# Kernel optimization log

Hardware: AMD Instinct MI355X
Metric: run time of the kernel (lower is better)

The kernel has to match this reference:

```python
import jax, jax.numpy as jnp
import numpy as np

B, T = 2, 512
E, NH, HD, V, P, L, KER, BLOCK = 768, 12, 64, 256, 4, 4, 16, 512
SCALE = HD ** -0.5


def _ln(x, g, b, eps=1e-5):
    m = jnp.mean(x, -1, keepdims=True)
    v = jnp.mean((x - m) ** 2, -1, keepdims=True)
    return (x - m) * jax.lax.rsqrt(v + eps) * g + b


def _rope_tables(n):
    inv = 1.0 / (10000.0 ** (jnp.arange(0, HD, 2, dtype=jnp.float32) / HD))
    f = jnp.arange(n, dtype=jnp.float32)[:, None] * inv[None, :]
    return jnp.cos(f), jnp.sin(f)


def _rope(x, cos, sin):
    # rotate over last two dims (positions, HD); split-half RoPE as in source
    h = x.shape[-1] // 2
    x1, x2 = x[..., :h], x[..., h:]
    return jnp.concatenate([x1 * cos - x2 * sin, x1 * sin + x2 * cos], axis=-1)


def _patch_attn(x, qkv_w, S):
    # x: [B,T,E]; sliding-window patch attention, step=1
    Bb, Tt, _ = x.shape
    q, k, v = jnp.split(x @ qkv_w, 3, axis=-1)
    heads = lambda t: t.reshape(Bb, Tt, NH, HD).transpose(0, 2, 1, 3)  # [B,NH,T,HD]
    q, k, v = heads(q), heads(k), heads(v)
    cos, sin = _rope_tables(Tt)
    q = _rope(q, cos, sin)
    k = _rope(k, cos, sin)
    # prefix: full causal attention over first S tokens
    sc = jnp.einsum('bnqh,bnkh->bnqk', q[:, :, :S], k[:, :, :S]) * SCALE
    mask = jnp.tril(jnp.ones((S, S), dtype=bool))
    sc = jnp.where(mask, sc, jnp.float32(-jnp.inf))
    out = jnp.einsum('bnqk,bnkh->bnqh', jax.nn.softmax(sc, axis=-1), v[:, :, :S])
    if Tt > S:
        # query t (t>=S) attends keys [t-S+1, t] (mask_sliding is all-ones for step=1)
        idx = jnp.arange(Tt - S)[:, None] + 1 + jnp.arange(S)[None, :]  # [T-S,S]
        kw = k[:, :, idx]  # [B,NH,T-S,S,HD]
        vw = v[:, :, idx]
        qs = q[:, :, S:]   # [B,NH,T-S,HD]
        sw = jnp.einsum('bnth,bntsh->bnts', qs, kw) * SCALE
        ow = jnp.einsum('bnts,bntsh->bnth', jax.nn.softmax(sw, axis=-1), vw)
        out = jnp.concatenate([out, ow], axis=2)
    return out.transpose(0, 2, 1, 3).reshape(Bb, Tt, NH * HD)


def _sa_block(x, ln0g, ln0b, ln1g, ln1b, qkv_w, proj_w, proj_b, w1, b1, w2, b2):
    # x: [B,T,P,V]; full (unmasked) attention over the P prediction slots
    Bb, Tt, Pp, _ = x.shape
    h = _ln(x, ln0g, ln0b)
    q, k, v = jnp.split(h @ qkv_w, 3, axis=-1)
    heads = lambda t: t.reshape(Bb, Tt, Pp, NH, HD).transpose(0, 1, 3, 2, 4)  # [B,T,NH,P,HD]
    q, k, v = heads(q), heads(k), heads(v)
    cos, sin = _rope_tables(Pp)
    q = _rope(q, cos, sin)
    k = _rope(k, cos, sin)
    sc = jnp.einsum('btnph,btnqh->btnpq', q, k) * SCALE
    o = jnp.einsum('btnpq,btnqh->btnph', jax.nn.softmax(sc, axis=-1), v)
    o = o.transpose(0, 1, 3, 2, 4).reshape(Bb, Tt, Pp, NH * HD)
    x = x + (o @ proj_w + proj_b)
    h2 = _ln(x, ln1g, ln1b)
    ff = jax.nn.gelu(h2 @ w1 + b1, approximate=False) @ w2 + b2
    return x + ff


def _forward(tokens, emb, blk_ln0_g, blk_ln0_b, blk_ln1_g, blk_ln1_b, blk_qkv_w,
             blk_ff_w1, blk_ff_b1, blk_ff_w2, blk_ff_b2, fin_ln_g, fin_ln_b,
             head_w, head_b, sa_ln0_g, sa_ln0_b, sa_ln1_g, sa_ln1_b, sa_qkv_w,
             sa_proj_w, sa_proj_b, sa_ff_w1, sa_ff_b1, sa_ff_w2, sa_ff_b2):
    x0 = emb[tokens]  # [B,T,E]
    x = x0
    for i in range(L):
        S = min(KER * 2 ** i, BLOCK)
        h = _ln(x, blk_ln0_g[i], blk_ln0_b[i])
        x = x + _patch_attn(h, blk_qkv_w[i], S)
        h2 = _ln(x, blk_ln1_g[i], blk_ln1_b[i])
        x = x + (jax.nn.gelu(h2 @ blk_ff_w1[i] + blk_ff_b1[i], approximate=False)
                 @ blk_ff_w2[i] + blk_ff_b2[i])
    x = x0 + x  # Golu: x = token_embedding(x); x = x + blocks(x)
    x = _ln(x, fin_ln_g, fin_ln_b)
    logits = (x @ head_w + head_b).reshape(B, T, P, V)
    logits = _sa_block(logits, sa_ln0_g, sa_ln0_b, sa_ln1_g, sa_ln1_b, sa_qkv_w,
                       sa_proj_w, sa_proj_b, sa_ff_w1, sa_ff_b1, sa_ff_w2, sa_ff_b2)
    return logits[:, :, 0, :]  # [B,T,V] (y is None path)


def setup_inputs() -> dict:
    key = jax.random.key(0)
    ks = jax.random.split(key, 12)
    w = lambda k, sh: jax.random.normal(k, sh, dtype=jnp.float32) * 0.02
    return {
        'tokens': jax.random.randint(ks[0], (B, T), 0, V),
        'emb': w(ks[1], (V, E)),
        'blk_ln0_g': jnp.ones((L, E), jnp.float32),
        'blk_ln0_b': jnp.zeros((L, E), jnp.float32),
        'blk_ln1_g': jnp.ones((L, E), jnp.float32),
        'blk_ln1_b': jnp.zeros((L, E), jnp.float32),
        'blk_qkv_w': w(ks[2], (L, E, 3 * E)),
        'blk_ff_w1': w(ks[3], (L, E, 4 * E)),
        'blk_ff_b1': jnp.zeros((L, 4 * E), jnp.float32),
        'blk_ff_w2': w(ks[4], (L, 4 * E, E)),
        'blk_ff_b2': jnp.zeros((L, E), jnp.float32),
        'fin_ln_g': jnp.ones((E,), jnp.float32),
        'fin_ln_b': jnp.zeros((E,), jnp.float32),
        'head_w': w(ks[5], (E, V * P)),
        'head_b': jnp.zeros((V * P,), jnp.float32),
        'sa_ln0_g': jnp.ones((V,), jnp.float32),
        'sa_ln0_b': jnp.zeros((V,), jnp.float32),
        'sa_ln1_g': jnp.ones((V,), jnp.float32),
        'sa_ln1_b': jnp.zeros((V,), jnp.float32),
        'sa_qkv_w': w(ks[6], (V, 3 * E)),
        'sa_proj_w': w(ks[7], (E, V)),
        'sa_proj_b': jnp.zeros((V,), jnp.float32),
        'sa_ff_w1': w(ks[8], (V, 4 * V)),
        'sa_ff_b1': jnp.zeros((4 * V,), jnp.float32),
        'sa_ff_w2': w(ks[9], (4 * V, V)),
        'sa_ff_b2': jnp.zeros((V,), jnp.float32),
    }


def reference(tokens, emb, blk_ln0_g, blk_ln0_b, blk_ln1_g, blk_ln1_b, blk_qkv_w,
              blk_ff_w1, blk_ff_b1, blk_ff_w2, blk_ff_b2, fin_ln_g, fin_ln_b,
              head_w, head_b, sa_ln0_g, sa_ln0_b, sa_ln1_g, sa_ln1_b, sa_qkv_w,
              sa_proj_w, sa_proj_b, sa_ff_w1, sa_ff_b1, sa_ff_w2, sa_ff_b2):
    return _forward(tokens, emb, blk_ln0_g, blk_ln0_b, blk_ln1_g, blk_ln1_b,
                    blk_qkv_w, blk_ff_w1, blk_ff_b1, blk_ff_w2, blk_ff_b2,
                    fin_ln_g, fin_ln_b, head_w, head_b, sa_ln0_g, sa_ln0_b,
                    sa_ln1_g, sa_ln1_b, sa_qkv_w, sa_proj_w, sa_proj_b,
                    sa_ff_w1, sa_ff_b1, sa_ff_w2, sa_ff_b2)
```

## Files before the change

kernel.cpp:

```cpp
#include <hip/hip_runtime.h>
#include <hip/hip_bf16.h>
#include <cstdint>
#include <cstddef>

#define BB    2
#define TSEQ  512
#define EDIM  768
#define NHEAD 12
#define HDIM  64
#define VDIM  256
#define PDIM  4
#define NROW  (BB*TSEQ)
#define NROW2 (BB*TSEQ*PDIM)

typedef __attribute__((ext_vector_type(8))) short short8;
typedef __attribute__((ext_vector_type(4))) short short4v;
typedef __attribute__((ext_vector_type(4))) float floatx4;

__device__ __forceinline__ float gelu_f(float v){
    return 0.5f * v * (1.0f + erff(v * 0.70710678118654752f));
}
__device__ __forceinline__ float b2f(short s){
    unsigned u = ((unsigned)(unsigned short)s) << 16;
    float f; __builtin_memcpy(&f, &u, 4); return f;
}
__device__ __forceinline__ short f2bs(float v){
    __hip_bfloat16 h = __float2bfloat16(v);
    short s; __builtin_memcpy(&s, &h, 2); return s;
}
__device__ __forceinline__ void gload16(const void* g, void* l){
    __builtin_amdgcn_global_load_lds((const __attribute__((address_space(1))) void*)g,
                                     (__attribute__((address_space(3))) void*)l, 16, 0, 0);
}

#define WAITN(n) asm volatile("s_waitcnt vmcnt(" #n ")" ::: "memory")
#define WAIT_STAGE(rem, full, half)                         \
    do{ if((rem) >= 2)      WAITN(full);                    \
        else if((rem) == 1) WAITN(half);                    \
        else                WAITN(0);                       \
        asm volatile("s_barrier" ::: "memory"); }while(0)
#define WAIT_STAGE8T(rem)                                   \
    do{ if((rem) >= 6)      WAITN(12);                      \
        else if((rem) == 5) WAITN(10);                      \
        else if((rem) == 4) WAITN(8);                       \
        else if((rem) == 3) WAITN(6);                       \
        else if((rem) == 2) WAITN(4);                       \
        else if((rem) == 1) WAITN(2);                       \
        else                WAITN(0);                       \
        asm volatile("s_barrier" ::: "memory"); }while(0)

struct WD2 { const float* in; __hip_bfloat16* out; int K; int N; int nt; };
struct WDs { WD2 d[17]; };

__global__ __launch_bounds__(256) void wconv_all(WDs a)
{
    int id = blockIdx.x;
    int i = 0;
    while(i < 16 && id >= a.d[i].nt){ id -= a.d[i].nt; i++; }
    WD2 w = a.d[i];
    const int tx = w.N / 128;
    const int n0 = (id % tx) * 128, k0 = (id / tx) * 128;
    __shared__ short t[128*128];
    {
        const int c4 = (threadIdx.x & 31) * 4;
        const int r0 = threadIdx.x >> 5;
        #pragma unroll
        for(int half = 0; half < 2; half++){
            float4 v[8];
            #pragma unroll
            for(int it = 0; it < 8; it++){
                int r = r0 + it*8 + half*64;
                v[it] = *(const float4*)(w.in + (size_t)(k0 + r) * w.N + n0 + c4);
            }
            #pragma unroll
            for(int it = 0; it < 8; it++){
                int r = r0 + it*8 + half*64;
                int nswz = c4 ^ (((r >> 3) & 15) << 2);
                short4v o;
                o[0] = f2bs(v[it].x); o[1] = f2bs(v[it].y);
                o[2] = f2bs(v[it].z); o[3] = f2bs(v[it].w);
                *(short4v*)&t[r*128 + nswz] = o;
            }
        }
    }
    __syncthreads();
    {
        const int k8 = (threadIdx.x & 15) * 8;
        const int nr = threadIdx.x >> 4;
        const int swz = (k8 >> 3) << 2;
        #pragma unroll
        for(int pass = 0; pass < 8; pass++){
            int n = nr + pass*16;
            int nswz = n ^ swz;
            short8 o;
            #pragma unroll
            for(int j = 0; j < 8; j++) o[j] = t[(k8 + j)*128 + nswz];
            *(short8*)((short*)w.out + (size_t)(n0 + n) * w.K + k0 + k8) = o;
        }
    }
}

template<int EPI>
__global__ __launch_bounds__(256) void gemm64q(
    const short* __restrict__ A, const short* __restrict__ Bt,
    const float* __restrict__ bias, __hip_bfloat16* __restrict__ Cout,
    __hip_bfloat16* __restrict__ qrb, __hip_bfloat16* __restrict__ krb,
    __hip_bfloat16* __restrict__ vvb,
    const float* __restrict__ rc, const float* __restrict__ rs,
    int M, int N, int K)
{
    alignas(16) __shared__ short As[4*64*32];
    alignas(16) __shared__ short Bs[4*64*32];
    const int tid  = threadIdx.x;
    const int lane = tid & 63;
    const int wave = tid >> 6;
    const int bm = blockIdx.y * 64, bn = blockIdx.x * 64;
    const int wm = wave * 16;
    const int quad = lane >> 4, l16 = lane & 15;

    floatx4 acc[4];
    #pragma unroll
    for(int j = 0; j < 4; j++) acc[j] = floatx4{0.f, 0.f, 0.f, 0.f};

    const int r  = tid >> 2;
    const int c8 = (tid & 3) * 8;
    const int ldsoff = (tid & 192) * 16;

    auto issue = [&](int k0, int cur){
        char* ab = (char*)As + cur*4096 + ldsoff;
        char* bb = (char*)Bs + cur*4096 + ldsoff;
        gload16(A  + (size_t)(bm + r) * K + k0 + c8, ab);
        gload16(Bt + (size_t)(bn + r) * K + k0 + c8, bb);
    };

    const int niter = K >> 5;
    issue(0, 0); issue(32, 1); issue(64, 2);
    for(int it = 0; it < niter; it++){
        WAIT_STAGE(niter - 1 - it, 4, 2);
        if(it + 3 < niter) issue((it + 3) << 5, (it + 3) & 3);
        const short* Ab = As + (it & 3) * 2048;
        const short* Bb = Bs + (it & 3) * 2048;
        short8 af = *(const short8*)&Ab[(wm + l16)*32 + quad*8];
        short8 bfr[4];
        #pragma unroll
        for(int j = 0; j < 4; j++)
            bfr[j] = *(const short8*)&Bb[(j*16 + l16)*32 + quad*8];
        #pragma unroll
        for(int j = 0; j < 4; j++)
            acc[j] = __builtin_amdgcn_mfma_f32_16x16x32_bf16(af, bfr[j], acc[j], 0, 0, 0);
    }

    if(EPI == 2){
        const int region = bn / 768;
        const int h = (bn % 768) >> 6;
        #pragma unroll
        for(int rr = 0; rr < 4; rr++){
            int row = bm + wm + quad*4 + rr;
            int t = row & (TSEQ-1), b = row >> 9;
            float a0 = acc[0][rr], a1 = acc[1][rr];
            float a2 = acc[2][rr], a3 = acc[3][rr];
            size_t dbase = ((size_t)(b*NHEAD + h)*TSEQ + t)*HDIM;
            if(region == 2){
                vvb[dbase + l16]      = __float2bfloat16(a0);
                vvb[dbase + 16 + l16] = __float2bfloat16(a1);
                vvb[dbase + 32 + l16] = __float2bfloat16(a2);
                vvb[dbase + 48 + l16] = __float2bfloat16(a3);
            }else{
                float c0 = rc[t*32 + l16],      s0 = rs[t*32 + l16];
                float c1 = rc[t*32 + 16 + l16], s1 = rs[t*32 + 16 + l16];
                __hip_bfloat16* dst = (region == 0) ? qrb : krb;
                dst[dbase + l16]      = __float2bfloat16(a0*c0 - a2*s0);
                dst[dbase + 16 + l16] = __float2bfloat16(a1*c1 - a3*s1);
                dst[dbase + 32 + l16] = __float2bfloat16(a0*s0 + a2*c0);
                dst[dbase + 48 + l16] = __float2bfloat16(a1*s1 + a3*c1);
            }
        }
        return;
    }

    if(EPI == 3){
        const int region = bn / 768;
        #pragma unroll
        for(int rr = 0; rr < 4; rr++){
            int row = bm + wm + quad*4 + rr;
            float a0 = acc[0][rr], a1 = acc[1][rr];
            float a2 = acc[2][rr], a3 = acc[3][rr];
            size_t rowb = (size_t)row * N + bn;
            if(region == 2){
                Cout[rowb + l16]      = __float2bfloat16(a0);
                Cout[rowb + 16 + l16] = __float2bfloat16(a1);
                Cout[rowb + 32 + l16] = __float2bfloat16(a2);
                Cout[rowb + 48 + l16] = __float2bfloat16(a3);
            }else{
                int p = row & 3;
                float c0 = rc[p*32 + l16],      s0 = rs[p*32 + l16];
                float c1 = rc[p*32 + 16 + l16], s1 = rs[p*32 + 16 + l16];
                Cout[rowb + l16]      = __float2bfloat16(a0*c0 - a2*s0);
                Cout[rowb + 16 + l16] = __float2bfloat16(a1*c1 - a3*s1);
                Cout[rowb + 32 + l16] = __float2bfloat16(a0*s0 + a2*c0);
                Cout[rowb + 48 + l16] = __float2bfloat16(a1*s1 + a3*c1);
            }
        }
        return;
    }

    #pragma unroll
    for(int j = 0; j < 4; j++){
        int col = bn + j*16 + l16;
        float bv = bias ? bias[col] : 0.f;
        #pragma unroll
        for(int rr = 0; rr < 4; rr++){
            int row = bm + wm + quad*4 + rr;
            float v = acc[j][rr] + bv;
            v = gelu_f(v);
            Cout[(size_t)row * N + col] = __float2bfloat16(v);
        }
    }
}

template<int RESID, int OUTC>
__global__ __launch_bounds__(256) void gemm64t(
    const short* __restrict__ A, const short* __restrict__ Bt,
    const float* __restrict__ bias, const float* __restrict__ resid,
    float* __restrict__ Cf, float* __restrict__ outp, int M, int N, int K)
{
    alignas(16) __shared__ short As[8*64*32];
    alignas(16) __shared__ short Bs[8*64*32];
    const int tid  = threadIdx.x;
    const int lane = tid & 63;
    const int wave = tid >> 6;
    const int bm = blockIdx.y * 64, bn = blockIdx.x * 64;
    const int wm = (wave >> 1) * 32, wn = (wave & 1) * 32;
    const int quad = lane >> 4, l16 = lane & 15;

    floatx4 acc[2][2];
    #pragma unroll
    for(int i = 0; i < 2; i++)
        #pragma unroll
        for(int j = 0; j < 2; j++)
            acc[i][j] = floatx4{0.f, 0.f, 0.f, 0.f};

    const int r  = tid >> 2;
    const int c8 = (tid & 3) * 8;
    const int ldsoff = (tid & 192) * 16;

    auto issue = [&](int k0, int cur){
        char* ab = (char*)As + cur*4096 + ldsoff;
        char* bb = (char*)Bs + cur*4096 + ldsoff;
        gload16(A  + (size_t)(bm + r) * K + k0 + c8, ab);
        gload16(Bt + (size_t)(bn + r) * K + k0 + c8, bb);
    };

    const int niter = K >> 5;
    issue(0, 0); issue(32, 1); issue(64, 2); issue(96, 3);
    issue(128, 4); issue(160, 5); issue(192, 6);
    for(int it = 0; it < niter; it++){
        WAIT_STAGE8T(niter - 1 - it);
        if(it + 7 < niter) issue((it + 7) << 5, (it + 7) & 7);
        const short* Ab = As + (it & 7) * 2048;
        const short* Bb = Bs + (it & 7) * 2048;
        short8 af[2], bfr[2];
        #pragma unroll
        for(int i = 0; i < 2; i++){
            af[i]  = *(const short8*)&Ab[(wm + i*16 + l16)*32 + quad*8];
            bfr[i] = *(const short8*)&Bb[(wn + i*16 + l16)*32 + quad*8];
        }
        #pragma unroll
        for(int i = 0; i < 2; i++)
            #pragma unroll
            for(int j = 0; j < 2; j++)
                acc[i][j] = __builtin_amdgcn_mfma_f32_16x16x32_bf16(af[i], bfr[j], acc[i][j], 0, 0, 0);
    }

    #pragma unroll
    for(int i = 0; i < 2; i++){
        int row0 = bm + wm + i*16 + quad*4;
        #pragma unroll
        for(int j = 0; j < 2; j++){
            int col = bn + wn + j*16 + l16;
            float bv = bias ? bias[col] : 0.f;
            #pragma unroll
            for(int rr = 0; rr < 4; rr++){
                int row = row0 + rr;
                float v = acc[i][j][rr] + bv;
                if(RESID) v += resid[(size_t)row * N + col];
                Cf[(size_t)row * N + col] = v;
                if(OUTC && (row & 3) == 0)
                    outp[(size_t)(row >> 2) * N + col] = v;
            }
        }
    }
}

template<int D>
__global__ __launch_bounds__(256) void ln_wave(
    const float* __restrict__ in, const float* __restrict__ in2,
    const float* __restrict__ g, const float* __restrict__ bta,
    __hip_bfloat16* __restrict__ out)
{
    constexpr int NC = D / 256;
    const int row  = blockIdx.x * 4 + (threadIdx.x >> 6);
    const int lane = threadIdx.x & 63;
    const float* xr = in + (size_t)row * D;
    float4 v[NC];
    float sum = 0.f, sq = 0.f;
    #pragma unroll
    for(int j = 0; j < NC; j++){
        int d0 = (lane + 64*j) * 4;
        v[j] = *(const float4*)(xr + d0);
        if(in2){
            float4 u = *(const float4*)(in2 + (size_t)row * D + d0);
            v[j].x += u.x; v[j].y += u.y; v[j].z += u.z; v[j].w += u.w;
        }
        sum += v[j].x + v[j].y + v[j].z + v[j].w;
        sq  += v[j].x*v[j].x + v[j].y*v[j].y + v[j].z*v[j].z + v[j].w*v[j].w;
    }
    #pragma unroll
    for(int off = 32; off > 0; off >>= 1){
        sum += __shfl_xor(sum, off, 64);
        sq  += __shfl_xor(sq,  off, 64);
    }
    const float m    = sum / D;
    const float rstd = rsqrtf(fmaxf(sq / D - m*m, 0.f) + 1e-5f);
    #pragma unroll
    for(int j = 0; j < NC; j++){
        int d0 = (lane + 64*j) * 4;
        float4 gg = *(const float4*)(g + d0);
        float4 bb = *(const float4*)(bta + d0);
        short4v o;
        o[0] = f2bs((v[j].x - m) * rstd * gg.x + bb.x);
        o[1] = f2bs((v[j].y - m) * rstd * gg.y + bb.y);
        o[2] = f2bs((v[j].z - m) * rstd * gg.z + bb.z);
        o[3] = f2bs((v[j].w - m) * rstd * gg.w + bb.w);
        *(short4v*)((short*)out + (size_t)row * D + d0) = o;
    }
}

__global__ __launch_bounds__(256) void embed_rope(
    const int* __restrict__ tokens, const float* __restrict__ emb,
    float* __restrict__ x0, float* __restrict__ x,
    float* __restrict__ rc, float* __restrict__ rs)
{
    const int blk = blockIdx.x;
    if(blk < NROW){
        const int tok = tokens[blk];
        const float4* src = (const float4*)(emb + (size_t)tok * EDIM);
        float4* d0 = (float4*)(x0 + (size_t)blk * EDIM);
        float4* d1 = (float4*)(x  + (size_t)blk * EDIM);
        if(threadIdx.x < EDIM/4){
            float4 v = src[threadIdx.x]; d0[threadIdx.x] = v; d1[threadIdx.x] = v;
        }
        return;
    }
    int i = (blk - NROW) * 256 + threadIdx.x;
    int pos = i >> 5, d = i & 31;
    float inv = powf(10000.0f, -(float)(2*d) / 64.0f);
    float f = (float)pos * inv;
    rc[i] = cosf(f);
    rs[i] = sinf(f);
}

template<int S>
__global__ __launch_bounds__(256) void patch_attn16(
    const __hip_bfloat16* __restrict__ qr, const __hip_bfloat16* __restrict__ kr,
    const __hip_bfloat16* __restrict__ vv, float* __restrict__ x)
{
    constexpr int W = S + 15;
    alignas(16) __shared__ short Ks[W*64];
    alignas(16) __shared__ short Vs[W*64];
    __shared__ float qlds[16*64];
    __shared__ float pb[16*128];

    const int t0 = blockIdx.x * 16;
    const int h = blockIdx.y, b = blockIdx.z;
    const int tid = threadIdx.x;
    const int wv = tid >> 6, lane = tid & 63;
    const size_t headbase = ((size_t)(b*NHEAD + h)) * TSEQ;

    const int c = tid & 7;
    for(int r = tid >> 3; r < W; r += 32){
        int g = t0 - S + 1 + r;
        int gc = g < 0 ? 0 : g;
        int sc = (c ^ (r & 7)) * 8;
        *(short8*)&Ks[r*64 + sc] = *(const short8*)((const short*)kr + (headbase + gc)*64 + c*8);
        *(short8*)&Vs[r*64 + sc] = *(const short8*)((const short*)vv + (headbase + gc)*64 + c*8);
    }
    for(int i = tid; i < 16*64; i += 256)
        qlds[i] = __bfloat162float(qr[(headbase + t0 + (i >> 6))*64 + (i & 63)]);
    __syncthreads();

    #pragma unroll
    for(int qq = 0; qq < 4; qq++){
        const int ql = wv*4 + qq;
        const int t  = t0 + ql;
        const int r0 = (S >= 64) ? (ql + lane) : ((lane < S) ? (ql + lane) : 0);
        const int r1 = ql + lane + 64;
        float a0 = 0.f, a1 = 0.f;
        #pragma unroll
        for(int ch = 0; ch < 8; ch++){
            float4 qa = *(const float4*)&qlds[ql*64 + ch*8];
            float4 qb = *(const float4*)&qlds[ql*64 + ch*8 + 4];
            short8 k0 = *(const short8*)&Ks[r0*64 + ((ch ^ (r0 & 7))*8)];
            a0 += qa.x*b2f(k0[0]) + qa.y*b2f(k0[1]) + qa.z*b2f(k0[2]) + qa.w*b2f(k0[3])
                + qb.x*b2f(k0[4]) + qb.y*b2f(k0[5]) + qb.z*b2f(k0[6]) + qb.w*b2f(k0[7]);
            if(S == 128){
                short8 k1 = *(const short8*)&Ks[r1*64 + ((ch ^ (r1 & 7))*8)];
                a1 += qa.x*b2f(k1[0]) + qa.y*b2f(k1[1]) + qa.z*b2f(k1[2]) + qa.w*b2f(k1[3])
                    + qb.x*b2f(k1[4]) + qb.y*b2f(k1[5]) + qb.z*b2f(k1[6]) + qb.w*b2f(k1[7]);
            }
        }
        const int key0 = t - S + 1 + lane;
        const bool v0 = (lane < S) && (key0 >= 0);
        const bool v1 = (S == 128) && (key0 + 64 >= 0);
        float s0 = v0 ? a0 * 0.125f : -1e30f;
        float s1 = v1 ? a1 * 0.125f : -1e30f;
        float mx = fmaxf(s0, s1);
        #pragma unroll
        for(int off = 32; off > 0; off >>= 1) mx = fmaxf(mx, __shfl_xor(mx, off, 64));
        float p0 = v0 ? expf(s0 - mx) : 0.f;
        float p1 = v1 ? expf(s1 - mx) : 0.f;
        float sm = p0 + p1;
        #pragma unroll
        for(int off = 32; off > 0; off >>= 1) sm += __shfl_xor(sm, off, 64);
        const float inv = 1.f / sm;
        pb[ql*128 + lane] = p0 * inv;
        if(S == 128) pb[ql*128 + lane + 64] = p1 * inv;
    }

    const int d = lane;
    const int coff = d >> 3, dlo = d & 7;
    #pragma unroll
    for(int qq = 0; qq < 4; qq++){
        const int ql = wv*4 + qq;
        float o = 0.f;
        #pragma unroll 8
        for(int j = 0; j < S; j++){
            int r = ql + j;
            float p = pb[ql*128 + j];
            o += p * b2f(Vs[r*64 + ((coff ^ (r & 7))*8) + dlo]);
        }
        x[((size_t)(b*TSEQ) + t0 + ql) * EDIM + h*HDIM + d] += o;
    }
}

__global__ __launch_bounds__(256) void sa_attn(
    const __hip_bfloat16* __restrict__ qkv2, __hip_bfloat16* __restrict__ o)
{
    const int t = blockIdx.x, h = blockIdx.y, b = blockIdx.z;
    const int p = threadIdx.x >> 6, lane = threadIdx.x & 63;
    const int row0 = (b*TSEQ + t) * PDIM;
    const short* base = (const short*)qkv2 + (size_t)row0 * (3*EDIM);
    const int d = lane;
    float q = b2f(base[(size_t)p*(3*EDIM) + h*HDIM + d]);
    float sc[4];
    #pragma unroll
    for(int j = 0; j < 4; j++){
        float kj = b2f(base[(size_t)j*(3*EDIM) + EDIM + h*HDIM + d]);
        float v = q * kj;
        #pragma unroll
        for(int off = 32; off > 0; off >>= 1) v += __shfl_xor(v, off, 64);
        sc[j] = v * 0.125f;
    }
    float m = fmaxf(fmaxf(sc[0], sc[1]), fmaxf(sc[2], sc[3]));
    float e0 = expf(sc[0]-m), e1 = expf(sc[1]-m), e2 = expf(sc[2]-m), e3 = expf(sc[3]-m);
    float idn = 1.f / (e0 + e1 + e2 + e3);
    float ov = (e0 * b2f(base[0*(3*EDIM) + 2*EDIM + h*HDIM + d])
              + e1 * b2f(base[1*(3*EDIM) + 2*EDIM + h*HDIM + d])
              + e2 * b2f(base[2*(3*EDIM) + 2*EDIM + h*HDIM + d])
              + e3 * b2f(base[3*(3*EDIM) + 2*EDIM + h*HDIM + d])) * idn;
    o[(size_t)(row0 + p) * EDIM + h*HDIM + d] = __float2bfloat16(ov);
}

extern "C" void kernel_launch(void* const* d_in, const int* in_sizes, int n_in,
                              void* d_out, int out_size, void* d_ws, size_t ws_size,
                              hipStream_t stream)
{
    const int*   tokens    = (const int*)  d_in[0];
    const float* emb       = (const float*)d_in[1];
    const float* bl0g      = (const float*)d_in[2];
    const float* bl0b      = (const float*)d_in[3];
    const float* bl1g      = (const float*)d_in[4];
    const float* bl1b      = (const float*)d_in[5];
    const float* qkv_w     = (const float*)d_in[6];
    const float* ff_w1     = (const float*)d_in[7];
    const float* ff_b1     = (const float*)d_in[8];
    const float* ff_w2     = (const float*)d_in[9];
    const float* ff_b2     = (const float*)d_in[10];
    const float* fin_g     = (const float*)d_in[11];
    const float* fin_b     = (const float*)d_in[12];
    const float* head_w    = (const float*)d_in[13];
    const float* head_b    = (const float*)d_in[14];
    const float* sa_ln0_g  = (const float*)d_in[15];
    const float* sa_ln0_b  = (const float*)d_in[16];
    const float* sa_ln1_g  = (const float*)d_in[17];
    const float* sa_ln1_b  = (const float*)d_in[18];
    const float* sa_qkv_w  = (const float*)d_in[19];
    const float* sa_proj_w = (const float*)d_in[20];
    const float* sa_proj_b = (const float*)d_in[21];
    const float* sa_ff_w1  = (const float*)d_in[22];
    const float* sa_ff_b1  = (const float*)d_in[23];
    const float* sa_ff_w2  = (const float*)d_in[24];
    const float* sa_ff_b2  = (const float*)d_in[25];
    float* out = (float*)d_out;

    char* p = (char*)d_ws;
    auto alloc = [&](size_t bytes){ char* q = p; p += (bytes + 255) & ~(size_t)255; return q; };

    float* logits = (float*)alloc((size_t)NROW2*VDIM*4);
    float* ropec  = (float*)alloc(512*32*4);
    float* ropes  = (float*)alloc(512*32*4);
    __hip_bfloat16* wqkvT[4]; for(int i=0;i<4;i++) wqkvT[i] = (__hip_bfloat16*)alloc((size_t)768*2304*2);
    __hip_bfloat16* wff1T[4]; for(int i=0;i<4;i++) wff1T[i] = (__hip_bfloat16*)alloc((size_t)768*3072*2);
    __hip_bfloat16* wff2T[4]; for(int i=0;i<4;i++) wff2T[i] = (__hip_bfloat16*)alloc((size_t)3072*768*2);
    __hip_bfloat16* wheadT   = (__hip_bfloat16*)alloc((size_t)768*1024*2);
    __hip_bfloat16* wsaqkvT  = (__hip_bfloat16*)alloc((size_t)256*2304*2);
    __hip_bfloat16* wsaprojT = (__hip_bfloat16*)alloc((size_t)768*256*2);
    __hip_bfloat16* wsaff1T  = (__hip_bfloat16*)alloc((size_t)256*1024*2);
    __hip_bfloat16* wsaff2T  = (__hip_bfloat16*)alloc((size_t)1024*256*2);
    char* U = p;
    float* x0           = (float*)(U);
    float* x            = (float*)(U + 3145728);
    __hip_bfloat16* h   = (__hip_bfloat16*)(U + 6291456);
    __hip_bfloat16* ff1 = (__hip_bfloat16*)(U + 7864320);
    __hip_bfloat16* qrb = (__hip_bfloat16*)(U + 14155776);
    __hip_bfloat16* krb = (__hip_bfloat16*)(U + 15728640);
    __hip_bfloat16* vvb = (__hip_bfloat16*)(U + 17301504);
    __hip_bfloat16* h2    = (__hip_bfloat16*)(U);
    __hip_bfloat16* qkv2  = (__hip_bfloat16*)(U + 2097152);
    __hip_bfloat16* sa_o  = (__hip_bfloat16*)(U + 20971520);
    __hip_bfloat16* sa_f1 = (__hip_bfloat16*)(U + 27262976);

    embed_rope<<<NROW + 64, 256, 0, stream>>>(tokens, emb, x0, x, ropec, ropes);
    {
        WDs wds; int tot = 0, n = 0;
        auto add = [&](const float* in, __hip_bfloat16* o2, int K, int N){
            wds.d[n++] = WD2{in, o2, K, N, (N/128)*(K/128)};
            tot += (N/128)*(K/128);
        };
        for(int i=0;i<4;i++){
            add(qkv_w + (size_t)i*768*2304, wqkvT[i], 768, 2304);
            add(ff_w1 + (size_t)i*768*3072, wff1T[i], 768, 3072);
            add(ff_w2 + (size_t)i*3072*768, wff2T[i], 3072, 768);
        }
        add(head_w,    wheadT,   768, 1024);
        add(sa_qkv_w,  wsaqkvT,  256, 2304);
        add(sa_proj_w, wsaprojT, 768, 256);
        add(sa_ff_w1,  wsaff1T,  256, 1024);
        add(sa_ff_w2,  wsaff2T, 1024, 256);
        wconv_all<<<tot, 256, 0, stream>>>(wds);
    }

    for(int i = 0; i < 4; i++){
        ln_wave<EDIM><<<NROW/4, 256, 0, stream>>>(x, nullptr, bl0g + i*EDIM, bl0b + i*EDIM, h);
        gemm64q<2><<<dim3(36, 16), 256, 0, stream>>>(
            (const short*)h, (const short*)wqkvT[i], nullptr, nullptr,
            qrb, krb, vvb, ropec, ropes, NROW, 3*EDIM, EDIM);
        dim3 agrid(TSEQ/16, NHEAD, BB);
        if(i == 0)      patch_attn16<16><<<agrid, 256, 0, stream>>>(qrb, krb, vvb, x);
        else if(i == 1) patch_attn16<32><<<agrid, 256, 0, stream>>>(qrb, krb, vvb, x);
        else if(i == 2) patch_attn16<64><<<agrid, 256, 0, stream>>>(qrb, krb, vvb, x);
        else            patch_attn16<128><<<agrid, 256, 0, stream>>>(qrb, krb, vvb, x);
        ln_wave<EDIM><<<NROW/4, 256, 0, stream>>>(x, nullptr, bl1g + i*EDIM, bl1b + i*EDIM, h);
        gemm64q<1><<<dim3(48, 16), 256, 0, stream>>>(
            (const short*)h, (const short*)wff1T[i], ff_b1 + (size_t)i*4*EDIM, ff1,
            nullptr, nullptr, nullptr, nullptr, nullptr, NROW, 4*EDIM, EDIM);
        gemm64t<1,0><<<dim3(12, 16), 256, 0, stream>>>(
            (const short*)ff1, (const short*)wff2T[i], ff_b2 + (size_t)i*EDIM, x, x, nullptr,
            NROW, EDIM, 4*EDIM);
    }

    ln_wave<EDIM><<<NROW/4, 256, 0, stream>>>(x, x0, fin_g, fin_b, h);
    gemm64t<0,0><<<dim3(16, 16), 256, 0, stream>>>(
        (const short*)h, (const short*)wheadT, head_b, nullptr, logits, nullptr,
        NROW, PDIM*VDIM, EDIM);

    ln_wave<VDIM><<<NROW2/4, 256, 0, stream>>>(logits, nullptr, sa_ln0_g, sa_ln0_b, h2);
    gemm64q<3><<<dim3(36, 64), 256, 0, stream>>>(
        (const short*)h2, (const short*)wsaqkvT, nullptr, qkv2,
        nullptr, nullptr, nullptr, ropec, ropes, NROW2, 3*EDIM, VDIM);
    sa_attn<<<dim3(TSEQ, NHEAD, BB), 256, 0, stream>>>(qkv2, sa_o);
    gemm64t<1,0><<<dim3(4, 64), 256, 0, stream>>>(
        (const short*)sa_o, (const short*)wsaprojT, sa_proj_b, logits, logits, nullptr,
        NROW2, VDIM, EDIM);
    ln_wave<VDIM><<<NROW2/4, 256, 0, stream>>>(logits, nullptr, sa_ln1_g, sa_ln1_b, h2);
    gemm64q<1><<<dim3(16, 64), 256, 0, stream>>>(
        (const short*)h2, (const short*)wsaff1T, sa_ff_b1, sa_f1,
        nullptr, nullptr, nullptr, nullptr, nullptr, NROW2, 4*VDIM, VDIM);
    gemm64t<1,1><<<dim3(4, 64), 256, 0, stream>>>(
        (const short*)sa_f1, (const short*)wsaff2T, sa_ff_b2, logits, logits, out,
        NROW2, VDIM, 4*VDIM);
}
```

Measured before the change: 707.5 us.

## Share V row loads across four queries in patch attention and shrink GEMM pipeline

```diff
diff --git a/kernel.cpp b/kernel.cpp
--- a/kernel.cpp
+++ b/kernel.cpp
@@ -37,15 +37,6 @@
 #define WAIT_STAGE(rem, full, half)                         \
     do{ if((rem) >= 2)      WAITN(full);                    \
         else if((rem) == 1) WAITN(half);                    \
-        else                WAITN(0);                       \
-        asm volatile("s_barrier" ::: "memory"); }while(0)
-#define WAIT_STAGE8T(rem)                                   \
-    do{ if((rem) >= 6)      WAITN(12);                      \
-        else if((rem) == 5) WAITN(10);                      \
-        else if((rem) == 4) WAITN(8);                       \
-        else if((rem) == 3) WAITN(6);                       \
-        else if((rem) == 2) WAITN(4);                       \
-        else if((rem) == 1) WAITN(2);                       \
         else                WAITN(0);                       \
         asm volatile("s_barrier" ::: "memory"); }while(0)
 
@@ -224,8 +215,8 @@
     const float* __restrict__ bias, const float* __restrict__ resid,
     float* __restrict__ Cf, float* __restrict__ outp, int M, int N, int K)
 {
-    alignas(16) __shared__ short As[8*64*32];
-    alignas(16) __shared__ short Bs[8*64*32];
+    alignas(16) __shared__ short As[4*64*32];
+    alignas(16) __shared__ short Bs[4*64*32];
     const int tid  = threadIdx.x;
     const int lane = tid & 63;
     const int wave = tid >> 6;
@@ -252,13 +243,12 @@
     };
 
     const int niter = K >> 5;
-    issue(0, 0); issue(32, 1); issue(64, 2); issue(96, 3);
-    issue(128, 4); issue(160, 5); issue(192, 6);
+    issue(0, 0); issue(32, 1); issue(64, 2);
     for(int it = 0; it < niter; it++){
-        WAIT_STAGE8T(niter - 1 - it);
-        if(it + 7 < niter) issue((it + 7) << 5, (it + 7) & 7);
-        const short* Ab = As + (it & 7) * 2048;
-        const short* Bb = Bs + (it & 7) * 2048;
+        WAIT_STAGE(niter - 1 - it, 4, 2);
+        if(it + 3 < niter) issue((it + 3) << 5, (it + 3) & 3);
+        const short* Ab = As + (it & 3) * 2048;
+        const short* Bb = Bs + (it & 3) * 2048;
         short8 af[2], bfr[2];
         #pragma unroll
         for(int i = 0; i < 2; i++){
@@ -366,10 +356,11 @@
     const __hip_bfloat16* __restrict__ vv, float* __restrict__ x)
 {
     constexpr int W = S + 15;
+    constexpr int PBW = S + 8;
     alignas(16) __shared__ short Ks[W*64];
     alignas(16) __shared__ short Vs[W*64];
     __shared__ float qlds[16*64];
-    __shared__ float pb[16*128];
+    __shared__ float pb[16*PBW];
 
     const int t0 = blockIdx.x * 16;
     const int h = blockIdx.y, b = blockIdx.z;
@@ -423,24 +414,36 @@
         #pragma unroll
         for(int off = 32; off > 0; off >>= 1) sm += __shfl_xor(sm, off, 64);
         const float inv = 1.f / sm;
-        pb[ql*128 + lane] = p0 * inv;
-        if(S == 128) pb[ql*128 + lane + 64] = p1 * inv;
+        if(lane < S) pb[ql*PBW + 4 + lane] = p0 * inv;
+        if(S == 128) pb[ql*PBW + 4 + 64 + lane] = p1 * inv;
+        if(lane < 4){
+            pb[ql*PBW + lane] = 0.f;
+            pb[ql*PBW + 4 + S + lane] = 0.f;
+        }
     }
 
     const int d = lane;
     const int coff = d >> 3, dlo = d & 7;
-    #pragma unroll
-    for(int qq = 0; qq < 4; qq++){
-        const int ql = wv*4 + qq;
-        float o = 0.f;
-        #pragma unroll 8
-        for(int j = 0; j < S; j++){
-            int r = ql + j;
-            float p = pb[ql*128 + j];
-            o += p * b2f(Vs[r*64 + ((coff ^ (r & 7))*8) + dlo]);
-        }
-        x[((size_t)(b*TSEQ) + t0 + ql) * EDIM + h*HDIM + d] += o;
-    }
+    const int rb = wv*4;
+    const int p0b = (rb+0)*PBW + 4;
+    const int p1b = (rb+1)*PBW + 3;
+    const int p2b = (rb+2)*PBW + 2;
+    const int p3b = (rb+3)*PBW + 1;
+    float o0 = 0.f, o1 = 0.f, o2 = 0.f, o3 = 0.f;
+    #pragma unroll 8
+    for(int rr = 0; rr <= S + 2; rr++){
+        int r = rb + rr;
+        float v = b2f(Vs[r*64 + ((coff ^ (r & 7))*8) + dlo]);
+        o0 += pb[p0b + rr] * v;
+        o1 += pb[p1b + rr] * v;
+        o2 += pb[p2b + rr] * v;
+        o3 += pb[p3b + rr] * v;
+    }
+    float* xp = x + ((size_t)(b*TSEQ) + t0 + rb) * EDIM + h*HDIM + d;
+    xp[0*EDIM] += o0;
+    xp[1*EDIM] += o1;
+    xp[2*EDIM] += o2;
+    xp[3*EDIM] += o3;
 }
 
 __global__ __launch_bounds__(256) void sa_attn(
```

Result: faster. 661.5 us (-6.5%).
